# Kernel optimization log

Measured on AMD Instinct MI355X. Metric: run time of the kernel, lower is better.

## Reference

```python
import jax, jax.numpy as jnp
import numpy as np

N_NODES = 50000
N_EDGES = 800000
N_LABEL = 200000
IN_DIM = 64
HID = 64
NEG_SLOPE = 0.2  # PyG GATConv default
EPS = 1e-16      # PyG softmax denominator eps


def _gat_conv(x, edge_index, edge_attr, W, att_src, att_dst, We, att_edge, bias):
    """PyG GATConv, heads=1, concat=True, add_self_loops=False, edge_dim=1."""
    n = x.shape[0]
    h = x @ W  # [N, H]
    src, dst = edge_index[0], edge_index[1]
    # per-edge attention logits
    alpha = (h @ att_src)[src] + (h @ att_dst)[dst] + (edge_attr @ We) @ att_edge  # [E]
    alpha = jax.nn.leaky_relu(alpha, NEG_SLOPE)
    # softmax over incoming edges of each dst node
    amax = jax.ops.segment_max(alpha, dst, num_segments=n)
    p = jnp.exp(alpha - amax[dst])
    denom = jax.ops.segment_sum(p, dst, num_segments=n)
    coef = p / (denom[dst] + EPS)  # [E]
    # weighted scatter-aggregate of source features
    out = jax.ops.segment_sum(h[src] * coef[:, None], dst, num_segments=n)
    return out + bias


def setup_inputs() -> dict:
    key = jax.random.key(0)
    ks = jax.random.split(key, 20)
    s = 0.05
    inp = {
        "x": jax.random.normal(ks[0], (N_NODES, IN_DIM), dtype=jnp.float32),
        "edge_attr": jax.random.normal(ks[1], (N_EDGES, 1), dtype=jnp.float32),
        "author_W": jax.random.normal(ks[2], (IN_DIM, HID), dtype=jnp.float32) * s,
        "author_b": jnp.zeros((HID,), dtype=jnp.float32),
        "c1_W": jax.random.normal(ks[3], (HID, HID), dtype=jnp.float32) * s,
        "c1_as": jax.random.normal(ks[4], (HID,), dtype=jnp.float32) * s,
        "c1_ad": jax.random.normal(ks[5], (HID,), dtype=jnp.float32) * s,
        "c1_We": jax.random.normal(ks[6], (1, HID), dtype=jnp.float32) * s,
        "c1_ae": jax.random.normal(ks[7], (HID,), dtype=jnp.float32) * s,
        "c1_b": jnp.zeros((HID,), dtype=jnp.float32),
        "c2_W": jax.random.normal(ks[8], (HID, HID), dtype=jnp.float32) * s,
        "c2_as": jax.random.normal(ks[9], (HID,), dtype=jnp.float32) * s,
        "c2_ad": jax.random.normal(ks[10], (HID,), dtype=jnp.float32) * s,
        "c2_We": jax.random.normal(ks[11], (1, HID), dtype=jnp.float32) * s,
        "c2_ae": jax.random.normal(ks[12], (HID,), dtype=jnp.float32) * s,
        "c2_b": jnp.zeros((HID,), dtype=jnp.float32),
        "edge_index": jax.random.randint(ks[13], (2, N_EDGES), 0, N_NODES, dtype=jnp.int32),
        "edge_label_index": jax.random.randint(ks[14], (2, N_LABEL), 0, N_NODES, dtype=jnp.int32),
    }
    return inp


def reference(x, edge_attr, author_W, author_b,
              c1_W, c1_as, c1_ad, c1_We, c1_ae, c1_b,
              c2_W, c2_as, c2_ad, c2_We, c2_ae, c2_b,
              edge_index, edge_label_index):
    h = x @ author_W + author_b                                   # author_lin
    h = jax.nn.relu(_gat_conv(h, edge_index, edge_attr,
                              c1_W, c1_as, c1_ad, c1_We, c1_ae, c1_b))
    h = _gat_conv(h, edge_index, edge_attr,
                  c2_W, c2_as, c2_ad, c2_We, c2_ae, c2_b)
    # edge-wise dot-product classifier
    return (h[edge_label_index[0]] * h[edge_label_index[1]]).sum(axis=-1)
```

## Files before the change

kernel.cpp:

```cpp
#include <hip/hip_runtime.h>

#define N_NODES 50000
#define N_EDGES 800000
#define N_LABEL 200000
#define HID 64
#define SCAN_BLOCKS 196

static const size_t OFF_W1C  = 0;
static const size_t OFF_B1C  = 4096;
static const size_t OFF_CE   = 4160;
static const size_t OFF_H    = 4224;
static const size_t OFF_AGG  = OFF_H    + (size_t)N_NODES * HID;
static const size_t OFF_ASRC = OFF_AGG  + (size_t)N_NODES * HID;
static const size_t OFF_ADST = OFF_ASRC + (size_t)N_NODES;
static const size_t OFF_ROW  = OFF_ADST + (size_t)N_NODES;
static const size_t OFF_CNT  = OFF_ROW  + (size_t)N_NODES + 2;
static const size_t OFF_PACK = OFF_CNT  + (size_t)N_NODES;
static const size_t OFF_BSUM = OFF_PACK + 2 * (size_t)N_EDGES;

__global__ void prep_kernel(const float* __restrict__ Wa, const float* __restrict__ ba,
                            const float* __restrict__ c1W,
                            const float* __restrict__ c1We, const float* __restrict__ c1ae,
                            const float* __restrict__ c2We, const float* __restrict__ c2ae,
                            float* __restrict__ W1c, float* __restrict__ b1c,
                            float* __restrict__ ce) {
    int t = threadIdx.x;
    for (int idx = t; idx < 64 * 64; idx += 256) {
        int i = idx >> 6, j = idx & 63;
        float s = 0.f;
        for (int k = 0; k < 64; ++k) s += Wa[i * 64 + k] * c1W[k * 64 + j];
        W1c[idx] = s;
    }
    if (t < 64) {
        float s = 0.f;
        for (int k = 0; k < 64; ++k) s += ba[k] * c1W[k * 64 + t];
        b1c[t] = s;
    }
    if (t == 64) {
        float s = 0.f;
        for (int k = 0; k < 64; ++k) s += c1We[k] * c1ae[k];
        ce[0] = s;
    }
    if (t == 65) {
        float s = 0.f;
        for (int k = 0; k < 64; ++k) s += c2We[k] * c2ae[k];
        ce[1] = s;
    }
}

__global__ void hist_kernel(const int* __restrict__ ei, int* __restrict__ cnt) {
    int e = blockIdx.x * blockDim.x + threadIdx.x;
    if (e < N_EDGES) atomicAdd(&cnt[ei[N_EDGES + e]], 1);
}

__global__ void block_sum_kernel(const int* __restrict__ cnt, int* __restrict__ bsum) {
    __shared__ int red[256];
    int t = threadIdx.x;
    int i = blockIdx.x * 256 + t;
    red[t] = (i < N_NODES) ? cnt[i] : 0;
    __syncthreads();
    for (int off = 128; off > 0; off >>= 1) {
        if (t < off) red[t] += red[t + off];
        __syncthreads();
    }
    if (t == 0) bsum[blockIdx.x] = red[0];
}

__global__ void scan_bsum_kernel(int* __restrict__ bsum) {
    __shared__ int s[256];
    int t = threadIdx.x;
    int v = (t < SCAN_BLOCKS) ? bsum[t] : 0;
    s[t] = v;
    __syncthreads();
    for (int off = 1; off < 256; off <<= 1) {
        int u = (t >= off) ? s[t - off] : 0;
        __syncthreads();
        s[t] += u;
        __syncthreads();
    }
    if (t < SCAN_BLOCKS) bsum[t] = s[t] - v;
}

__global__ void scan_final_kernel(const int* __restrict__ cnt,
                                  const int* __restrict__ bsum,
                                  int* __restrict__ row_ptr) {
    __shared__ int s[256];
    int t = threadIdx.x;
    int i = blockIdx.x * 256 + t;
    int v = (i < N_NODES) ? cnt[i] : 0;
    s[t] = v;
    __syncthreads();
    for (int off = 1; off < 256; off <<= 1) {
        int u = (t >= off) ? s[t - off] : 0;
        __syncthreads();
        s[t] += u;
        __syncthreads();
    }
    int excl = s[t] - v + bsum[blockIdx.x];
    if (i < N_NODES) row_ptr[i] = excl;
    if (i == N_NODES - 1) row_ptr[N_NODES] = excl + v;
}

__global__ void scatter_kernel(const int* __restrict__ ei, const float* __restrict__ ea,
                               const int* __restrict__ row_ptr, int* __restrict__ cnt,
                               int2* __restrict__ pack) {
    int e = blockIdx.x * blockDim.x + threadIdx.x;
    if (e >= N_EDGES) return;
    int d = ei[N_EDGES + e];
    int old = atomicSub(&cnt[d], 1);
    int pos = row_ptr[d] + old - 1;
    int2 pr; pr.x = ei[e]; pr.y = __float_as_int(ea[e]);
    pack[pos] = pr;
}

__global__ void gemm_attn_kernel(const float* __restrict__ X,
                                 const float* __restrict__ W,
                                 const float* __restrict__ postb, int has_postb,
                                 const float* __restrict__ avs,
                                 const float* __restrict__ avd,
                                 float* __restrict__ H,
                                 float* __restrict__ Asrc, float* __restrict__ Adst) {
    int lane = threadIdx.x & 63;
    int wid  = __builtin_amdgcn_readfirstlane(threadIdx.x >> 6);
    int gwave  = blockIdx.x * 4 + wid;
    int nwaves = gridDim.x * 4;
    float wcol[64];
#pragma unroll
    for (int k = 0; k < 64; ++k) wcol[k] = W[k * 64 + lane];
    float as_l = avs[lane], ad_l = avd[lane];
    float ob = has_postb ? postb[lane] : 0.f;
    for (int row = gwave; row < N_NODES; row += nwaves) {
        const float4* xr4 = (const float4*)(X + (size_t)row * 64);
        float acc = ob;
#pragma unroll
        for (int i = 0; i < 16; ++i) {
            float4 xq = xr4[i];
            acc = fmaf(xq.x, wcol[4 * i + 0], acc);
            acc = fmaf(xq.y, wcol[4 * i + 1], acc);
            acc = fmaf(xq.z, wcol[4 * i + 2], acc);
            acc = fmaf(xq.w, wcol[4 * i + 3], acc);
        }
        H[(size_t)row * 64 + lane] = acc;
        float s1 = acc * as_l, s2 = acc * ad_l;
#pragma unroll
        for (int off = 32; off > 0; off >>= 1) {
            s1 += __shfl_xor(s1, off);
            s2 += __shfl_xor(s2, off);
        }
        if (lane == 0) { Asrc[row] = s1; Adst[row] = s2; }
    }
}

__global__ void aggregate_csr_kernel(const int* __restrict__ row_ptr,
                                     const int2* __restrict__ pack,
                                     const float* __restrict__ Asrc,
                                     const float* __restrict__ Adst,
                                     const float* __restrict__ cep,
                                     const float* __restrict__ H,
                                     float* __restrict__ Agg,
                                     const float* __restrict__ obias, int do_relu) {
    int t    = threadIdx.x;
    int q    = t & 15;
    int sub  = (t >> 4) & 3;
    int wid  = t >> 6;
    int node = blockIdx.x * 4 + wid;
    if (node >= N_NODES) return;
    float ce = *cep;
    float ad = Adst[node];
    int beg = row_ptr[node], end = row_ptr[node + 1];
    float ax = 0.f, ay = 0.f, az = 0.f, aw = 0.f, accp = 0.f;
    for (int pos = beg + sub; pos < end; pos += 4) {
        int2  pr  = pack[pos];
        int   s   = pr.x;
        float ev  = __int_as_float(pr.y);
        float as_ = Asrc[s];
        float4 hv = *(const float4*)(H + (size_t)s * 64 + q * 4);
        float al = as_ + ad + ev * ce;
        al = al >= 0.f ? al : 0.2f * al;
        float p = __expf(al);
        ax += p * hv.x; ay += p * hv.y; az += p * hv.z; aw += p * hv.w;
        accp += p;
    }
    ax += __shfl_xor(ax, 16); ax += __shfl_xor(ax, 32);
    ay += __shfl_xor(ay, 16); ay += __shfl_xor(ay, 32);
    az += __shfl_xor(az, 16); az += __shfl_xor(az, 32);
    aw += __shfl_xor(aw, 16); aw += __shfl_xor(aw, 32);
    accp += __shfl_xor(accp, 16); accp += __shfl_xor(accp, 32);
    if (sub == 0) {
        float inv = 1.f / (accp + 1e-16f);
        float4 o; o.x = ax * inv; o.y = ay * inv; o.z = az * inv; o.w = aw * inv;
        if (obias) {
            float4 b = ((const float4*)obias)[q];
            o.x += b.x; o.y += b.y; o.z += b.z; o.w += b.w;
            if (do_relu) {
                o.x = fmaxf(o.x, 0.f); o.y = fmaxf(o.y, 0.f);
                o.z = fmaxf(o.z, 0.f); o.w = fmaxf(o.w, 0.f);
            }
        }
        *(float4*)(Agg + (size_t)node * 64 + q * 4) = o;
    }
}

__global__ void classify_kernel(const int* __restrict__ eli,
                                const float* __restrict__ Agg,
                                const float* __restrict__ bias,
                                float* __restrict__ out) {
    int t    = threadIdx.x;
    int q    = t & 15;
    int grp  = (blockIdx.x * blockDim.x + t) >> 4;
    if (grp >= N_LABEL) return;
    int e = grp;
    float4 b = ((const float4*)bias)[q];
    int i = eli[e], j = eli[N_LABEL + e];
    float4 a = ((const float4*)(Agg + (size_t)i * 64))[q];
    float4 c = ((const float4*)(Agg + (size_t)j * 64))[q];
    float s = (a.x + b.x) * (c.x + b.x) + (a.y + b.y) * (c.y + b.y) +
              (a.z + b.z) * (c.z + b.z) + (a.w + b.w) * (c.w + b.w);
#pragma unroll
    for (int off = 8; off > 0; off >>= 1) s += __shfl_xor(s, off);
    if (q == 0) out[e] = s;
}

extern "C" void kernel_launch(void* const* d_in, const int* in_sizes, int n_in,
                              void* d_out, int out_size, void* d_ws, size_t ws_size,
                              hipStream_t stream) {
    const float* x    = (const float*)d_in[0];
    const float* ea   = (const float*)d_in[1];
    const float* Wa   = (const float*)d_in[2];
    const float* ba   = (const float*)d_in[3];
    const float* c1W  = (const float*)d_in[4];
    const float* c1as = (const float*)d_in[5];
    const float* c1ad = (const float*)d_in[6];
    const float* c1We = (const float*)d_in[7];
    const float* c1ae = (const float*)d_in[8];
    const float* c1b  = (const float*)d_in[9];
    const float* c2W  = (const float*)d_in[10];
    const float* c2as = (const float*)d_in[11];
    const float* c2ad = (const float*)d_in[12];
    const float* c2We = (const float*)d_in[13];
    const float* c2ae = (const float*)d_in[14];
    const float* c2b  = (const float*)d_in[15];
    const int*   ei   = (const int*)d_in[16];
    const int*   eli  = (const int*)d_in[17];
    float* out = (float*)d_out;

    float* w    = (float*)d_ws;
    float* W1c  = w + OFF_W1C;
    float* b1c  = w + OFF_B1C;
    float* ce   = w + OFF_CE;
    float* H    = w + OFF_H;
    float* Agg  = w + OFF_AGG;
    float* Asrc = w + OFF_ASRC;
    float* Adst = w + OFF_ADST;
    int*   rowp = (int*)(w + OFF_ROW);
    int*   cnt  = (int*)(w + OFF_CNT);
    int2*  pack = (int2*)(w + OFF_PACK);
    int*   bsum = (int*)(w + OFF_BSUM);

    prep_kernel<<<1, 256, 0, stream>>>(Wa, ba, c1W, c1We, c1ae, c2We, c2ae,
                                       W1c, b1c, ce);
    hipMemsetAsync(cnt, 0, (size_t)N_NODES * sizeof(int), stream);
    hist_kernel<<<(N_EDGES + 255) / 256, 256, 0, stream>>>(ei, cnt);
    block_sum_kernel<<<SCAN_BLOCKS, 256, 0, stream>>>(cnt, bsum);
    scan_bsum_kernel<<<1, 256, 0, stream>>>(bsum);
    scan_final_kernel<<<SCAN_BLOCKS, 256, 0, stream>>>(cnt, bsum, rowp);
    scatter_kernel<<<(N_EDGES + 255) / 256, 256, 0, stream>>>(ei, ea, rowp, cnt, pack);

    gemm_attn_kernel<<<1024, 256, 0, stream>>>(x, W1c, b1c, 1,
                                               c1as, c1ad, H, Asrc, Adst);
    aggregate_csr_kernel<<<12500, 256, 0, stream>>>(rowp, pack, Asrc, Adst,
                                                    ce + 0, H, Agg, c1b, 1);

    gemm_attn_kernel<<<1024, 256, 0, stream>>>(Agg, c2W, nullptr, 0,
                                               c2as, c2ad, H, Asrc, Adst);
    aggregate_csr_kernel<<<12500, 256, 0, stream>>>(rowp, pack, Asrc, Adst,
                                                    ce + 1, H, Agg, nullptr, 0);

    classify_kernel<<<(N_LABEL * 16 + 255) / 256, 256, 0, stream>>>(eli, Agg, c2b, out);
}
```

Before: 337.0 us.

## Split CSR edge scatter into two-pass bucketed scatter for locality

```diff
diff --git a/kernel.cpp b/kernel.cpp
--- a/kernel.cpp
+++ b/kernel.cpp
@@ -5,6 +5,7 @@
 #define N_LABEL 200000
 #define HID 64
 #define SCAN_BLOCKS 196
+#define NBUCKET 1563
 
 static const size_t OFF_W1C  = 0;
 static const size_t OFF_B1C  = 4096;
@@ -17,6 +18,8 @@
 static const size_t OFF_CNT  = OFF_ROW  + (size_t)N_NODES + 2;
 static const size_t OFF_PACK = OFF_CNT  + (size_t)N_NODES;
 static const size_t OFF_BSUM = OFF_PACK + 2 * (size_t)N_EDGES;
+static const size_t OFF_BB   = OFF_BSUM + 256;
+static const size_t OFF_BT   = OFF_BB   + NBUCKET;
 
 __global__ void prep_kernel(const float* __restrict__ Wa, const float* __restrict__ ba,
                             const float* __restrict__ c1W,
@@ -101,16 +104,42 @@
     if (i == N_NODES - 1) row_ptr[N_NODES] = excl + v;
 }
 
-__global__ void scatter_kernel(const int* __restrict__ ei, const float* __restrict__ ea,
-                               const int* __restrict__ row_ptr, int* __restrict__ cnt,
-                               int2* __restrict__ pack) {
+__global__ void bbase_kernel(const int* __restrict__ row_ptr,
+                             int* __restrict__ bbase, int* __restrict__ btick) {
+    int b = blockIdx.x * blockDim.x + threadIdx.x;
+    if (b < NBUCKET) {
+        int n0 = b * 32;
+        bbase[b] = row_ptr[n0 < N_NODES ? n0 : N_NODES];
+        btick[b] = 0;
+    }
+}
+
+__global__ void bucket_scatter_kernel(const int* __restrict__ ei,
+                                      const float* __restrict__ ea,
+                                      const int* __restrict__ bbase,
+                                      int* __restrict__ btick,
+                                      int4* __restrict__ tmp) {
     int e = blockIdx.x * blockDim.x + threadIdx.x;
     if (e >= N_EDGES) return;
     int d = ei[N_EDGES + e];
+    int b = d >> 5;
+    int pos = bbase[b] + atomicAdd(&btick[b], 1);
+    int4 pr; pr.x = ei[e]; pr.y = d; pr.z = __float_as_int(ea[e]); pr.w = 0;
+    tmp[pos] = pr;
+}
+
+__global__ void final_scatter_kernel(const int4* __restrict__ tmp,
+                                     const int* __restrict__ row_ptr,
+                                     int* __restrict__ cnt,
+                                     int2* __restrict__ pack) {
+    int e = blockIdx.x * blockDim.x + threadIdx.x;
+    if (e >= N_EDGES) return;
+    int4 pr = tmp[e];
+    int d = pr.y;
     int old = atomicSub(&cnt[d], 1);
     int pos = row_ptr[d] + old - 1;
-    int2 pr; pr.x = ei[e]; pr.y = __float_as_int(ea[e]);
-    pack[pos] = pr;
+    int2 o; o.x = pr.x; o.y = pr.z;
+    pack[pos] = o;
 }
 
 __global__ void gemm_attn_kernel(const float* __restrict__ X,
@@ -256,6 +285,9 @@
     int*   cnt  = (int*)(w + OFF_CNT);
     int2*  pack = (int2*)(w + OFF_PACK);
     int*   bsum = (int*)(w + OFF_BSUM);
+    int*   bbas = (int*)(w + OFF_BB);
+    int*   btic = (int*)(w + OFF_BT);
+    int4*  tmp  = (int4*)(w + OFF_H);
 
     prep_kernel<<<1, 256, 0, stream>>>(Wa, ba, c1W, c1We, c1ae, c2We, c2ae,
                                        W1c, b1c, ce);
@@ -264,7 +296,11 @@
     block_sum_kernel<<<SCAN_BLOCKS, 256, 0, stream>>>(cnt, bsum);
     scan_bsum_kernel<<<1, 256, 0, stream>>>(bsum);
     scan_final_kernel<<<SCAN_BLOCKS, 256, 0, stream>>>(cnt, bsum, rowp);
-    scatter_kernel<<<(N_EDGES + 255) / 256, 256, 0, stream>>>(ei, ea, rowp, cnt, pack);
+    bbase_kernel<<<(NBUCKET + 255) / 256, 256, 0, stream>>>(rowp, bbas, btic);
+    bucket_scatter_kernel<<<(N_EDGES + 255) / 256, 256, 0, stream>>>(ei, ea, bbas,
+                                                                     btic, tmp);
+    final_scatter_kernel<<<(N_EDGES + 255) / 256, 256, 0, stream>>>(tmp, rowp,
+                                                                    cnt, pack);
 
     gemm_attn_kernel<<<1024, 256, 0, stream>>>(x, W1c, b1c, 1,
                                                c1as, c1ad, H, Asrc, Adst);
```

Result: slower. 475.3 us (+41.0%).

## Replace random CSR scatter with two-level bucketed partition then local placement

Applied to the files above, without the earlier changes.

```diff
diff --git a/kernel.cpp b/kernel.cpp
--- a/kernel.cpp
+++ b/kernel.cpp
@@ -5,6 +5,8 @@
 #define N_LABEL 200000
 #define HID 64
 #define SCAN_BLOCKS 196
+#define NBKT 196
+#define NBLK 391
 
 static const size_t OFF_W1C  = 0;
 static const size_t OFF_B1C  = 4096;
@@ -17,6 +19,8 @@
 static const size_t OFF_CNT  = OFF_ROW  + (size_t)N_NODES + 2;
 static const size_t OFF_PACK = OFF_CNT  + (size_t)N_NODES;
 static const size_t OFF_BSUM = OFF_PACK + 2 * (size_t)N_EDGES;
+static const size_t OFF_CM   = OFF_BSUM + 256;
+static const size_t OFF_OM   = OFF_CM   + (size_t)NBKT * NBLK;
 
 __global__ void prep_kernel(const float* __restrict__ Wa, const float* __restrict__ ba,
                             const float* __restrict__ c1W,
@@ -101,16 +105,80 @@
     if (i == N_NODES - 1) row_ptr[N_NODES] = excl + v;
 }
 
-__global__ void scatter_kernel(const int* __restrict__ ei, const float* __restrict__ ea,
-                               const int* __restrict__ row_ptr, int* __restrict__ cnt,
-                               int2* __restrict__ pack) {
-    int e = blockIdx.x * blockDim.x + threadIdx.x;
-    if (e >= N_EDGES) return;
-    int d = ei[N_EDGES + e];
-    int old = atomicSub(&cnt[d], 1);
-    int pos = row_ptr[d] + old - 1;
-    int2 pr; pr.x = ei[e]; pr.y = __float_as_int(ea[e]);
-    pack[pos] = pr;
+__global__ void blkhist_kernel(const int* __restrict__ ei, int* __restrict__ countM) {
+    __shared__ int lh[NBKT];
+    int t = threadIdx.x, blk = blockIdx.x;
+    if (t < NBKT) lh[t] = 0;
+    __syncthreads();
+    int base = blk * 2048;
+#pragma unroll
+    for (int i = 0; i < 8; ++i) {
+        int e = base + i * 256 + t;
+        if (e < N_EDGES) atomicAdd(&lh[ei[N_EDGES + e] >> 8], 1);
+    }
+    __syncthreads();
+    if (t < NBKT) countM[t * NBLK + blk] = lh[t];
+}
+
+__global__ void bucket_scan_kernel(const int* __restrict__ countM,
+                                   const int* __restrict__ row_ptr,
+                                   int* __restrict__ offM) {
+    __shared__ int s[256];
+    int b = blockIdx.x, t = threadIdx.x;
+    int i0 = 2 * t, i1 = 2 * t + 1;
+    int c0 = (i0 < NBLK) ? countM[b * NBLK + i0] : 0;
+    int c1 = (i1 < NBLK) ? countM[b * NBLK + i1] : 0;
+    int own = c0 + c1;
+    s[t] = own;
+    __syncthreads();
+    for (int off = 1; off < 256; off <<= 1) {
+        int u = (t >= off) ? s[t - off] : 0;
+        __syncthreads();
+        s[t] += u;
+        __syncthreads();
+    }
+    int excl = s[t] - own + row_ptr[b * 256];
+    if (i0 < NBLK) offM[b * NBLK + i0] = excl;
+    if (i1 < NBLK) offM[b * NBLK + i1] = excl + c0;
+}
+
+__global__ void partition_kernel(const int* __restrict__ ei,
+                                 const float* __restrict__ ea,
+                                 const int* __restrict__ offM,
+                                 int2* __restrict__ tmp) {
+    __shared__ int lcur[NBKT];
+    int t = threadIdx.x, blk = blockIdx.x;
+    if (t < NBKT) lcur[t] = offM[t * NBLK + blk];
+    __syncthreads();
+    int base = blk * 2048;
+#pragma unroll
+    for (int i = 0; i < 8; ++i) {
+        int e = base + i * 256 + t;
+        if (e < N_EDGES) {
+            int d = ei[N_EDGES + e];
+            int pos = atomicAdd(&lcur[d >> 8], 1);
+            int2 pr; pr.x = (d << 16) | ei[e]; pr.y = __float_as_int(ea[e]);
+            tmp[pos] = pr;
+        }
+    }
+}
+
+__global__ void place_kernel(const int2* __restrict__ tmp,
+                             const int* __restrict__ row_ptr,
+                             int* __restrict__ cnt,
+                             int2* __restrict__ pack) {
+    int b = blockIdx.x;
+    int beg = row_ptr[b * 256];
+    int endn = (b + 1) * 256; if (endn > N_NODES) endn = N_NODES;
+    int end = row_ptr[endn];
+    for (int pos = beg + threadIdx.x; pos < end; pos += blockDim.x) {
+        int2 pr = tmp[pos];
+        int d = ((unsigned)pr.x) >> 16;
+        int old = atomicSub(&cnt[d], 1);
+        int slot = row_ptr[d] + old - 1;
+        int2 o; o.x = pr.x & 0xFFFF; o.y = pr.y;
+        pack[slot] = o;
+    }
 }
 
 __global__ void gemm_attn_kernel(const float* __restrict__ X,
@@ -256,6 +324,9 @@
     int*   cnt  = (int*)(w + OFF_CNT);
     int2*  pack = (int2*)(w + OFF_PACK);
     int*   bsum = (int*)(w + OFF_BSUM);
+    int*   cm   = (int*)(w + OFF_CM);
+    int*   om   = (int*)(w + OFF_OM);
+    int2*  tmp  = (int2*)(w + OFF_H);
 
     prep_kernel<<<1, 256, 0, stream>>>(Wa, ba, c1W, c1We, c1ae, c2We, c2ae,
                                        W1c, b1c, ce);
@@ -264,7 +335,10 @@
     block_sum_kernel<<<SCAN_BLOCKS, 256, 0, stream>>>(cnt, bsum);
     scan_bsum_kernel<<<1, 256, 0, stream>>>(bsum);
     scan_final_kernel<<<SCAN_BLOCKS, 256, 0, stream>>>(cnt, bsum, rowp);
-    scatter_kernel<<<(N_EDGES + 255) / 256, 256, 0, stream>>>(ei, ea, rowp, cnt, pack);
+    blkhist_kernel<<<NBLK, 256, 0, stream>>>(ei, cm);
+    bucket_scan_kernel<<<NBKT, 256, 0, stream>>>(cm, rowp, om);
+    partition_kernel<<<NBLK, 256, 0, stream>>>(ei, ea, om, tmp);
+    place_kernel<<<NBKT, 256, 0, stream>>>(tmp, rowp, cnt, pack);
 
     gemm_attn_kernel<<<1024, 256, 0, stream>>>(x, W1c, b1c, 1,
                                                c1as, c1ad, H, Asrc, Adst);
```

Result: faster. 323.8 us (-3.9%).
